# Kernel optimization log

Measured on AMD Instinct MI355X. Metric: run time of the kernel, lower is better.

Reference implementation:

```python
import jax, jax.numpy as jnp
import numpy as np

# ---- dims (see shape_source) ----
B, S = 1, 2048
D_MODEL, H, HD, RD = 2048, 16, 128, 64   # head_dim=128 (pow2 for Hadamard), rope dim 64
QLR = KVLR = 1024                        # lora ranks = d_model // 2
TOPK = 512
BLK = 32                                 # fp8 act-quant block size
FP8_MAX = 448.0                          # float8_e4m3 max
EPS = 1e-6


def linear(x, w, b):
    return x @ w.T + b


def rms_norm(x, w):
    return x * jax.lax.rsqrt(jnp.mean(x * x, axis=-1, keepdims=True) + EPS) * w


def rope_cos_sin(pos, d):
    half = d // 2
    inv = 1.0 / (10000.0 ** (jnp.arange(half, dtype=jnp.float32) / half))
    ang = pos[:, None].astype(jnp.float32) * inv[None, :]  # (s, half)
    return jnp.cos(ang), jnp.sin(ang)


def apply_rope(x, cos, sin):
    # rotate-half RoPE; cos/sin pre-broadcast to x's leading dims
    half = x.shape[-1] // 2
    x1, x2 = x[..., :half], x[..., half:]
    return jnp.concatenate([x1 * cos - x2 * sin, x2 * cos + x1 * sin], axis=-1)


def fwht(x):
    # fast Walsh-Hadamard transform over last dim (power of 2), scaled by d^-0.5
    d = x.shape[-1]
    lead = x.shape[:-1]
    h = 1
    while h < d:
        x = x.reshape(lead + (d // (2 * h), 2, h))
        x = jnp.concatenate([x[..., 0, :] + x[..., 1, :], x[..., 0, :] - x[..., 1, :]], axis=-1)
        x = x.reshape(lead + (d,))
        h *= 2
    return x * (d ** -0.5)


def act_quant_dequant(x):
    # block-scaled fp8 fake-quant: per-32-elem block, ue8m0 (power-of-2) scale, clamp to e4m3 range
    lead, d = x.shape[:-1], x.shape[-1]
    xb = x.reshape(lead + (d // BLK, BLK))
    amax = jnp.max(jnp.abs(xb), axis=-1)
    scale = jnp.exp2(jnp.ceil(jnp.log2(jnp.maximum(amax / FP8_MAX, 1e-12))))
    q = jnp.clip(xb / scale[..., None], -FP8_MAX, FP8_MAX)
    return (q * scale[..., None]).reshape(lead + (d,))


def setup_inputs() -> dict:
    key = jax.random.key(0)
    ks = iter(jax.random.split(key, 48))
    def W(o, i):
        return jax.random.normal(next(ks), (o, i), jnp.float32) * (i ** -0.5)
    def Bv(o):
        return jnp.zeros((o,), jnp.float32)
    return dict(
        x=jax.random.normal(next(ks), (B, S, D_MODEL), jnp.float32),
        start_pos=0,
        q_down_w=W(QLR, D_MODEL), q_down_b=Bv(QLR),
        q_norm_w=jnp.ones((QLR,), jnp.float32),
        q_nope_up_w=W(H * HD, QLR), q_nope_up_b=Bv(H * HD),
        q_rope_up_w=W(H * RD, QLR), q_rope_up_b=Bv(H * RD),
        kv_down_w=W(KVLR, D_MODEL), kv_down_b=Bv(KVLR),
        kv_norm_w=jnp.ones((KVLR,), jnp.float32),
        k_up_w=W(H * HD, KVLR), k_up_b=Bv(H * HD),
        v_up_w=W(H * HD, KVLR), v_up_b=Bv(H * HD),
        k_rope_w=W(RD, D_MODEL), k_rope_b=Bv(RD),
        out_w=W(D_MODEL, H * HD), out_b=Bv(D_MODEL),
        idx_q_w=W(H * HD, QLR), idx_q_b=Bv(H * HD),
        idx_k_w=W(HD, D_MODEL), idx_k_b=Bv(HD),
        idx_k_norm_w=jnp.ones((HD,), jnp.float32),
        idx_w_w=W(H, D_MODEL), idx_w_b=Bv(H),
    )


def reference(x, start_pos, q_down_w, q_down_b, q_norm_w, q_nope_up_w, q_nope_up_b,
              q_rope_up_w, q_rope_up_b, kv_down_w, kv_down_b, kv_norm_w,
              k_up_w, k_up_b, v_up_w, v_up_b, k_rope_w, k_rope_b, out_w, out_b,
              idx_q_w, idx_q_b, idx_k_w, idx_k_b, idx_k_norm_w, idx_w_w, idx_w_b):
    b, s, _ = x.shape
    pos = jnp.arange(start_pos, start_pos + s)
    cos_r, sin_r = rope_cos_sin(pos, RD)  # (s, RD/2)

    # --- MLA queries: low-rank down, RMSNorm, decoupled nope/rope up-proj ---
    q_c = rms_norm(linear(x, q_down_w, q_down_b), q_norm_w)            # (b,s,QLR)
    q_nope = linear(q_c, q_nope_up_w, q_nope_up_b).reshape(b, s, H, HD)
    q_rope = linear(q_c, q_rope_up_w, q_rope_up_b).reshape(b, s, H, RD)
    q_rope = apply_rope(q_rope, cos_r[:, None, :], sin_r[:, None, :])
    q = jnp.concatenate([q_nope, q_rope], axis=-1).transpose(0, 2, 1, 3)  # (b,H,s,HD+RD)

    # --- MLA keys/values: compressed kv + shared rope key ---
    kv_c = rms_norm(linear(x, kv_down_w, kv_down_b), kv_norm_w)        # (b,s,KVLR)
    k_pe = apply_rope(linear(x, k_rope_w, k_rope_b), cos_r, sin_r)     # (b,s,RD)
    k_nope = linear(kv_c, k_up_w, k_up_b).reshape(b, s, H, HD)
    v = linear(kv_c, v_up_w, v_up_b).reshape(b, s, H, HD).transpose(0, 2, 1, 3)
    k = jnp.concatenate(
        [k_nope, jnp.broadcast_to(k_pe[:, :, None, :], (b, s, H, RD))], axis=-1
    ).transpose(0, 2, 1, 3)                                            # (b,H,s,HD+RD)

    # --- lightning indexer: rotated, block-fp8-quantized scoring + top-k ---
    qi = linear(q_c, idx_q_w, idx_q_b).reshape(b, s, H, HD)
    ki = rms_norm(linear(x, idx_k_w, idx_k_b), idx_k_norm_w)           # (b,s,HD)
    qi_r = apply_rope(qi[..., :RD], cos_r[:, None, :], sin_r[:, None, :])
    ki_r = apply_rope(ki[..., :RD], cos_r, sin_r)
    qi = fwht(jnp.concatenate([qi[..., RD:], qi_r], axis=-1))          # rotate_activation
    ki = fwht(jnp.concatenate([ki[..., RD:], ki_r], axis=-1))
    qdq = act_quant_dequant(qi)                                        # (b,s,H,HD)
    kdq = act_quant_dequant(ki)                                        # (b,s,HD)
    w_idx = (x @ idx_w_w.T + idx_w_b) * (H ** -0.5)                    # (b,s,H)
    dots = jnp.einsum('bshd,btd->bsht', qdq, kdq)
    score = jnp.einsum('bsht,bsh->bst', jax.nn.relu(dots), w_idx) * (HD ** -0.5)
    _, topk_idx = jax.lax.top_k(score, min(TOPK, s))                   # (b,s,k)

    bi = jnp.arange(b)[:, None, None]
    si = jnp.arange(s)[None, :, None]
    index_mask = jnp.zeros((b, s, s), bool).at[bi, si, topk_idx].set(True)

    # --- sparse attention over selected tokens ---
    att = jnp.einsum('bhsd,bhtd->bhst', q, k) * ((HD + RD) ** -0.5)
    att = jnp.where(index_mask[:, None], att, jnp.float32(-1e30))
    att = jax.nn.softmax(att, axis=-1)
    o = jnp.einsum('bhst,bhtd->bhsd', att, v)
    o = o.transpose(0, 2, 1, 3).reshape(b, s, H * HD)
    return linear(o, out_w, out_b)
```

## Files before the change

kernel.cpp:

```cpp
#include <hip/hip_runtime.h>
#include <hip/hip_bf16.h>
#include <math.h>

#define S 2048
#define DM 2048
#define NH 16
#define HD 128
#define RD 64
#define LR 1024
#define TOPK 512

#define GT_M 128
#define GT_N 64
#define GT_K 16

__global__ __launch_bounds__(256)
void k_gemm(const float* __restrict__ A, const float* __restrict__ W,
            const float* __restrict__ bias, float* __restrict__ C,
            int M, int N, int K, float alpha)
{
    __shared__ float As[GT_K][GT_M + 4];
    __shared__ float Ws[GT_K][GT_N + 4];
    const int tid = threadIdx.x;
    const int tx = tid & 15, ty = tid >> 4;
    const int m0 = blockIdx.y * GT_M, n0 = blockIdx.x * GT_N;

    float acc[8][4];
#pragma unroll
    for (int i = 0; i < 8; ++i)
#pragma unroll
        for (int j = 0; j < 4; ++j) acc[i][j] = 0.f;

    const int ar = tid >> 1;
    const int ak = (tid & 1) << 3;
    const int wr = tid >> 2;
    const int wk = (tid & 3) << 2;

    for (int kk = 0; kk < K; kk += GT_K) {
        float4 v0 = *(const float4*)&A[(size_t)(m0 + ar) * K + kk + ak];
        float4 v1 = *(const float4*)&A[(size_t)(m0 + ar) * K + kk + ak + 4];
        float4 w0 = make_float4(0.f, 0.f, 0.f, 0.f);
        if (n0 + wr < N) w0 = *(const float4*)&W[(size_t)(n0 + wr) * K + kk + wk];
        __syncthreads();
        As[ak + 0][ar] = v0.x; As[ak + 1][ar] = v0.y; As[ak + 2][ar] = v0.z; As[ak + 3][ar] = v0.w;
        As[ak + 4][ar] = v1.x; As[ak + 5][ar] = v1.y; As[ak + 6][ar] = v1.z; As[ak + 7][ar] = v1.w;
        Ws[wk + 0][wr] = w0.x; Ws[wk + 1][wr] = w0.y; Ws[wk + 2][wr] = w0.z; Ws[wk + 3][wr] = w0.w;
        __syncthreads();
#pragma unroll
        for (int k = 0; k < GT_K; ++k) {
            float a0[8], b0[4];
            *(float4*)&a0[0] = *(const float4*)&As[k][ty * 8];
            *(float4*)&a0[4] = *(const float4*)&As[k][ty * 8 + 4];
            *(float4*)&b0[0] = *(const float4*)&Ws[k][tx * 4];
#pragma unroll
            for (int i = 0; i < 8; ++i)
#pragma unroll
                for (int j = 0; j < 4; ++j)
                    acc[i][j] = fmaf(a0[i], b0[j], acc[i][j]);
        }
    }
    const int n = n0 + tx * 4;
    if (n < N) {
#pragma unroll
        for (int i = 0; i < 8; ++i) {
            const int m = m0 + ty * 8 + i;
            float4 o;
            o.x = (acc[i][0] + bias[n + 0]) * alpha;
            o.y = (acc[i][1] + bias[n + 1]) * alpha;
            o.z = (acc[i][2] + bias[n + 2]) * alpha;
            o.w = (acc[i][3] + bias[n + 3]) * alpha;
            *(float4*)&C[(size_t)m * N + n] = o;
        }
    }
}

template<typename TA>
__global__ __launch_bounds__(256)
void k_gemm64(const TA* __restrict__ A, const float* __restrict__ W,
              const float* __restrict__ bias, double* __restrict__ C,
              int M, int N, int K, double alpha)
{
    __shared__ double As[16][66];
    __shared__ double Ws[16][66];
    const int tid = threadIdx.x;
    const int tx = tid & 15, ty = tid >> 4;
    const int m0 = blockIdx.y * 64, n0 = blockIdx.x * 64;
    const int r = tid >> 2, k4 = (tid & 3) << 2;

    double acc[4][4];
#pragma unroll
    for (int i = 0; i < 4; ++i)
#pragma unroll
        for (int j = 0; j < 4; ++j) acc[i][j] = 0.0;

    for (int kk = 0; kk < K; kk += 16) {
        double av[4], wv[4];
        const TA* ap = &A[(size_t)(m0 + r) * K + kk + k4];
#pragma unroll
        for (int i = 0; i < 4; ++i) av[i] = (double)ap[i];
        if (n0 + r < N) {
            const float* wp = &W[(size_t)(n0 + r) * K + kk + k4];
#pragma unroll
            for (int i = 0; i < 4; ++i) wv[i] = (double)wp[i];
        } else {
#pragma unroll
            for (int i = 0; i < 4; ++i) wv[i] = 0.0;
        }
        __syncthreads();
#pragma unroll
        for (int i = 0; i < 4; ++i) { As[k4 + i][r] = av[i]; Ws[k4 + i][r] = wv[i]; }
        __syncthreads();
#pragma unroll 4
        for (int k = 0; k < 16; ++k) {
            double a[4], b[4];
#pragma unroll
            for (int i = 0; i < 4; ++i) a[i] = As[k][ty * 4 + i];
#pragma unroll
            for (int j = 0; j < 4; ++j) b[j] = Ws[k][tx * 4 + j];
#pragma unroll
            for (int i = 0; i < 4; ++i)
#pragma unroll
                for (int j = 0; j < 4; ++j)
                    acc[i][j] = fma(a[i], b[j], acc[i][j]);
        }
    }
    const int n = n0 + tx * 4;
    if (n < N) {
#pragma unroll
        for (int i = 0; i < 4; ++i) {
            const int m = m0 + ty * 4 + i;
#pragma unroll
            for (int j = 0; j < 4; ++j)
                C[(size_t)m * N + n + j] = (acc[i][j] + (double)bias[n + j]) * alpha;
        }
    }
}

__global__ __launch_bounds__(256)
void k_rmsnorm(const float* __restrict__ X, const float* __restrict__ w,
               float* __restrict__ Y, int D)
{
    const int row = blockIdx.x;
    const float* x = X + (size_t)row * D;
    float* y = Y + (size_t)row * D;
    float ss = 0.f;
    for (int i = threadIdx.x; i < D; i += 256) { float v = x[i]; ss = fmaf(v, v, ss); }
#pragma unroll
    for (int m = 1; m < 64; m <<= 1) ss += __shfl_xor(ss, m, 64);
    __shared__ float red[4];
    if ((threadIdx.x & 63) == 0) red[threadIdx.x >> 6] = ss;
    __syncthreads();
    const float tot = red[0] + red[1] + red[2] + red[3];
    const float r = 1.0f / sqrtf(tot / (float)D + 1e-6f);
    for (int i = threadIdx.x; i < D; i += 256) y[i] = x[i] * r * w[i];
}

__global__ __launch_bounds__(256)
void k_rmsnorm64(const double* __restrict__ X, const float* __restrict__ w,
                 double* __restrict__ Y, int D)
{
    const int row = blockIdx.x;
    const double* x = X + (size_t)row * D;
    double* y = Y + (size_t)row * D;
    double ss = 0.0;
    for (int i = threadIdx.x; i < D; i += 256) { double v = x[i]; ss = fma(v, v, ss); }
#pragma unroll
    for (int m = 1; m < 64; m <<= 1) ss += __shfl_xor(ss, m, 64);
    __shared__ double red[4];
    if ((threadIdx.x & 63) == 0) red[threadIdx.x >> 6] = ss;
    __syncthreads();
    const double tot = red[0] + red[1] + red[2] + red[3];
    const double r = 1.0 / sqrt(tot / (double)D + 1e-6);
    for (int i = threadIdx.x; i < D; i += 256) y[i] = x[i] * r * (double)w[i];
}

__global__ __launch_bounds__(256)
void k_rope_table(const int* __restrict__ start_pos,
                  float* __restrict__ cos32, float* __restrict__ sin32)
{
    const int idx = blockIdx.x * 256 + threadIdx.x;
    if (idx >= S * 32) return;
    const int s = idx >> 5, j = idx & 31;
    const float posf = (float)(start_pos[0] + s);
    const double p64 = pow(10000.0, (double)j * 0.03125);
    const float p32 = (float)p64;
    const float inv32 = (float)(1.0 / (double)p32);
    const float ang = posf * inv32;
    cos32[idx] = (float)cos((double)ang);
    sin32[idx] = (float)sin((double)ang);
}

__global__ __launch_bounds__(256)
void k_rope_apply(float* __restrict__ X, const float* __restrict__ cosT,
                  const float* __restrict__ sinT, int heads)
{
    const int idx = blockIdx.x * 256 + threadIdx.x;
    if (idx >= S * heads * 32) return;
    const int j = idx & 31;
    const int vh = idx >> 5;
    const int s = vh / heads;
    const float c = cosT[s * 32 + j], sn = sinT[s * 32 + j];
    float* p = X + (size_t)vh * 64;
    const float x1 = p[j], x2 = p[32 + j];
    p[j]      = x1 * c - x2 * sn;
    p[32 + j] = x2 * c + x1 * sn;
}

__global__ __launch_bounds__(256)
void k_idx_prep64(double* __restrict__ X, const float* __restrict__ cosT,
                  const float* __restrict__ sinT, int heads, int nvec)
{
    const int wid = (int)((blockIdx.x * 256 + threadIdx.x) >> 6);
    const int lane = threadIdx.x & 63;
    if (wid >= nvec) return;
    const int s = wid / heads;
    double* x = X + (size_t)wid * 128;
    double y0, y1;
    if (lane < 32) {
        y0 = x[64 + 2 * lane]; y1 = x[64 + 2 * lane + 1];
    } else {
        const int j0 = (2 * (lane - 32)) & 31;
        const double a0 = x[j0], a1 = x[j0 + 1];
        const double b0 = x[j0 + 32], b1 = x[j0 + 33];
        const double c0 = (double)cosT[s * 32 + j0], c1 = (double)cosT[s * 32 + j0 + 1];
        const double s0 = (double)sinT[s * 32 + j0], s1 = (double)sinT[s * 32 + j0 + 1];
        if (lane < 48) { y0 = a0 * c0 - b0 * s0; y1 = a1 * c1 - b1 * s1; }
        else           { y0 = b0 * c0 + a0 * s0; y1 = b1 * c1 + a1 * s1; }
    }
    { const double t0 = y0 + y1, t1 = y0 - y1; y0 = t0; y1 = t1; }
#pragma unroll
    for (int m = 1; m < 64; m <<= 1) {
        const double p0 = __shfl_xor(y0, m, 64);
        const double p1 = __shfl_xor(y1, m, 64);
        if ((lane & m) == 0) { y0 = y0 + p0; y1 = y1 + p1; }
        else                 { y0 = p0 - y0; y1 = p1 - y1; }
    }
    const double SCL = 1.0 / sqrt(128.0);
    x[2 * lane] = y0 * SCL; x[2 * lane + 1] = y1 * SCL;
}

__global__ __launch_bounds__(256)
void k_score64(const double* __restrict__ QI, const double* __restrict__ KI,
               const double* __restrict__ Widx, double* __restrict__ SC)
{
    __shared__ double Qs[32][66];
    __shared__ double Ks[32][66];
    const int tid = threadIdx.x;
    const int tx = tid & 15, ty = tid >> 4;
    const int s0 = blockIdx.y * 64, t0 = blockIdx.x * 64;
    const int r = tid >> 2, k8 = (tid & 3) << 3;

    double sc[4][4];
#pragma unroll
    for (int i = 0; i < 4; ++i)
#pragma unroll
        for (int j = 0; j < 4; ++j) sc[i][j] = 0.0;

    for (int h = 0; h < NH; ++h) {
        double dot[4][4];
#pragma unroll
        for (int i = 0; i < 4; ++i)
#pragma unroll
            for (int j = 0; j < 4; ++j) dot[i][j] = 0.0;
        for (int kk = 0; kk < HD; kk += 32) {
            __syncthreads();
            {
                const double* qp = &QI[((size_t)(s0 + r) * NH + h) * HD + kk + k8];
                const double* kp = &KI[(size_t)(t0 + r) * HD + kk + k8];
#pragma unroll
                for (int i = 0; i < 8; ++i) { Qs[k8 + i][r] = qp[i]; Ks[k8 + i][r] = kp[i]; }
            }
            __syncthreads();
#pragma unroll 8
            for (int k = 0; k < 32; ++k) {
                double a[4], b[4];
#pragma unroll
                for (int i = 0; i < 4; ++i) a[i] = Qs[k][ty * 4 + i];
#pragma unroll
                for (int j = 0; j < 4; ++j) b[j] = Ks[k][tx * 4 + j];
#pragma unroll
                for (int i = 0; i < 4; ++i)
#pragma unroll
                    for (int j = 0; j < 4; ++j)
                        dot[i][j] = fma(a[i], b[j], dot[i][j]);
            }
        }
#pragma unroll
        for (int i = 0; i < 4; ++i) {
            const double w = Widx[(size_t)(s0 + ty * 4 + i) * NH + h];
#pragma unroll
            for (int j = 0; j < 4; ++j)
                sc[i][j] = fma(fmax(dot[i][j], 0.0), w, sc[i][j]);
        }
    }
    const double SCL = 1.0 / sqrt(128.0);
#pragma unroll
    for (int i = 0; i < 4; ++i)
#pragma unroll
        for (int j = 0; j < 4; ++j)
            SC[(size_t)(s0 + ty * 4 + i) * S + t0 + tx * 4 + j] = sc[i][j] * SCL;
}

__global__ __launch_bounds__(256)
void k_topk64(const double* __restrict__ SC, unsigned* __restrict__ Mask)
{
    __shared__ unsigned long long u[S];
    __shared__ int cnt_sh, cg_sh, ce_sh, cut_sh;
    const int tid = threadIdx.x;
    const int row = blockIdx.x;
    for (int j = tid; j < S; j += 256) {
        unsigned long long b = (unsigned long long)__double_as_longlong(SC[(size_t)row * S + j]);
        if (b == 0x8000000000000000ull) b = 0ull;
        u[j] = (b & 0x8000000000000000ull) ? ~b : (b | 0x8000000000000000ull);
    }
    __syncthreads();
    unsigned long long lo = 0ull, hi = ~0ull;
    for (int it = 0; it < 64 && lo < hi; ++it) {
        const unsigned long long mid = lo + ((hi - lo) >> 1) + 1ull;
        if (tid == 0) cnt_sh = 0;
        __syncthreads();
        int c = 0;
        for (int j = tid; j < S; j += 256) c += (u[j] >= mid) ? 1 : 0;
#pragma unroll
        for (int m = 1; m < 64; m <<= 1) c += __shfl_xor(c, m, 64);
        if ((tid & 63) == 0) atomicAdd(&cnt_sh, c);
        __syncthreads();
        const int cge = cnt_sh;
        __syncthreads();
        if (cge >= TOPK) lo = mid; else hi = mid - 1ull;
    }
    const unsigned long long T = lo;
    if (tid == 0) { cg_sh = 0; ce_sh = 0; }
    __syncthreads();
    int cg = 0, ce = 0;
    for (int j = tid; j < S; j += 256) {
        cg += (u[j] > T) ? 1 : 0; ce += (u[j] == T) ? 1 : 0;
    }
#pragma unroll
    for (int m = 1; m < 64; m <<= 1) { cg += __shfl_xor(cg, m, 64); ce += __shfl_xor(ce, m, 64); }
    if ((tid & 63) == 0) { atomicAdd(&cg_sh, cg); atomicAdd(&ce_sh, ce); }
    __syncthreads();
    if (tid == 0) {
        const int need = TOPK - cg_sh;
        int cut = S - 1;
        if (ce_sh != need) {
            int acc = 0; cut = -1;
            for (int t = 0; t < S; ++t)
                if (u[t] == T) { ++acc; if (acc == need) { cut = t; break; } }
        }
        cut_sh = cut;
    }
    __syncthreads();
    const int cut = cut_sh;
    for (int w = tid; w < S / 32; w += 256) {
        unsigned bits = 0u;
#pragma unroll 4
        for (int b = 0; b < 32; ++b) {
            const int j = w * 32 + b;
            const bool sel = (u[j] > T) || ((u[j] == T) && (j <= cut));
            bits |= (sel ? 1u : 0u) << b;
        }
        Mask[(size_t)row * (S / 32) + w] = bits;
    }
}

__global__ __launch_bounds__(256)
void k_attn(const float* __restrict__ QN, const float* __restrict__ QR,
            const float* __restrict__ KN, const float* __restrict__ KP,
            const float* __restrict__ V, const unsigned* __restrict__ Mask,
            float* __restrict__ O)
{
    __shared__ float AB[2 * 64 * 68];
    __shared__ float Ps[64][68];
    const int tid = threadIdx.x;
    const int tx = tid & 15, ty = tid >> 4;
    const int h = blockIdx.y;
    const int s0 = blockIdx.x * 64;
    const int r = tid >> 2;
    const int c4 = (tid & 3) << 2;

    float o[4][8];
    float mrow[4], lrow[4];
#pragma unroll
    for (int i = 0; i < 4; ++i) {
        mrow[i] = -INFINITY; lrow[i] = 0.f;
#pragma unroll
        for (int jd = 0; jd < 8; ++jd) o[i][jd] = 0.f;
    }

    for (int t0 = 0; t0 < S; t0 += 64) {
        float lg[4][4];
#pragma unroll
        for (int i = 0; i < 4; ++i)
#pragma unroll
            for (int j = 0; j < 4; ++j) lg[i][j] = 0.f;

        for (int c = 0; c < 3; ++c) {
            __syncthreads();
#pragma unroll
            for (int jj = 0; jj < 4; ++jj) {
                const int kk = c4 + 16 * jj;
                float4 va, vb;
                if (c < 2) {
                    va = *(const float4*)&QN[((size_t)(s0 + r) * NH + h) * HD + c * 64 + kk];
                    vb = *(const float4*)&KN[((size_t)(t0 + r) * NH + h) * HD + c * 64 + kk];
                } else {
                    va = *(const float4*)&QR[((size_t)(s0 + r) * NH + h) * RD + kk];
                    vb = *(const float4*)&KP[(size_t)(t0 + r) * RD + kk];
                }
                AB[(kk + 0) * 68 + r] = va.x; AB[(kk + 1) * 68 + r] = va.y;
                AB[(kk + 2) * 68 + r] = va.z; AB[(kk + 3) * 68 + r] = va.w;
                AB[4352 + (kk + 0) * 68 + r] = vb.x; AB[4352 + (kk + 1) * 68 + r] = vb.y;
                AB[4352 + (kk + 2) * 68 + r] = vb.z; AB[4352 + (kk + 3) * 68 + r] = vb.w;
            }
            __syncthreads();
#pragma unroll 16
            for (int k = 0; k < 64; ++k) {
                float a[4], b[4];
                *(float4*)a = *(const float4*)&AB[k * 68 + ty * 4];
                *(float4*)b = *(const float4*)&AB[4352 + k * 68 + tx * 4];
#pragma unroll
                for (int i = 0; i < 4; ++i)
#pragma unroll
                    for (int j = 0; j < 4; ++j)
                        lg[i][j] = fmaf(a[i], b[j], lg[i][j]);
            }
        }
        __syncthreads();

        float p[4][4], mt[4], alpha[4], psum[4];
#pragma unroll
        for (int i = 0; i < 4; ++i) {
            mt[i] = -INFINITY;
            const unsigned mw = Mask[(size_t)(s0 + 4 * ty + i) * (S / 32) + (t0 >> 5) + (tx >> 3)];
            const unsigned nib = (mw >> ((tx & 7) << 2)) & 0xFu;
#pragma unroll
            for (int j = 0; j < 4; ++j) {
                if ((nib >> j) & 1u) {
                    const float l = lg[i][j] * 0.07216878364870323f;
                    p[i][j] = l;
                    mt[i] = fmaxf(mt[i], l);
                } else p[i][j] = -INFINITY;
            }
        }
#pragma unroll
        for (int m = 1; m < 16; m <<= 1)
#pragma unroll
            for (int i = 0; i < 4; ++i) mt[i] = fmaxf(mt[i], __shfl_xor(mt[i], m, 64));
#pragma unroll
        for (int i = 0; i < 4; ++i) {
            const float mnew = fmaxf(mrow[i], mt[i]);
            alpha[i] = (mnew == -INFINITY) ? 1.f : expf(mrow[i] - mnew);
            mrow[i] = mnew;
            psum[i] = 0.f;
            float pj[4];
#pragma unroll
            for (int j = 0; j < 4; ++j) {
                const float pv = (p[i][j] == -INFINITY) ? 0.f : expf(p[i][j] - mnew);
                pj[j] = pv; psum[i] += pv;
            }
            *(float4*)&Ps[4 * ty + i][tx * 4] = make_float4(pj[0], pj[1], pj[2], pj[3]);
        }
#pragma unroll
        for (int m = 1; m < 16; m <<= 1)
#pragma unroll
            for (int i = 0; i < 4; ++i) psum[i] += __shfl_xor(psum[i], m, 64);
#pragma unroll
        for (int i = 0; i < 4; ++i) {
            lrow[i] = lrow[i] * alpha[i] + psum[i];
#pragma unroll
            for (int jd = 0; jd < 8; ++jd) o[i][jd] *= alpha[i];
        }
#pragma unroll
        for (int jj = 0; jj < 8; ++jj) {
            const int dq = c4 + 16 * jj;
            float4 vv = *(const float4*)&V[((size_t)(t0 + r) * NH + h) * HD + dq];
            AB[r * 128 + dq + 0] = vv.x; AB[r * 128 + dq + 1] = vv.y;
            AB[r * 128 + dq + 2] = vv.z; AB[r * 128 + dq + 3] = vv.w;
        }
        __syncthreads();
#pragma unroll 4
        for (int tc = 0; tc < 64; ++tc) {
            float pv[4];
#pragma unroll
            for (int i = 0; i < 4; ++i) pv[i] = Ps[4 * ty + i][tc];
#pragma unroll
            for (int jd = 0; jd < 8; ++jd) {
                const float vvv = AB[tc * 128 + tx + 16 * jd];
#pragma unroll
                for (int i = 0; i < 4; ++i) o[i][jd] = fmaf(pv[i], vvv, o[i][jd]);
            }
        }
    }
#pragma unroll
    for (int i = 0; i < 4; ++i) {
        const float inv = 1.0f / lrow[i];
#pragma unroll
        for (int jd = 0; jd < 8; ++jd)
            O[((size_t)(s0 + 4 * ty + i) * NH + h) * HD + tx + 16 * jd] = o[i][jd] * inv;
    }
}

__global__ __launch_bounds__(256)
void k_cast64to32(const double* __restrict__ X, float* __restrict__ Y, int n)
{
    const int i = blockIdx.x * 256 + threadIdx.x;
    if (i < n) Y[i] = (float)X[i];
}

extern "C" void kernel_launch(void* const* d_in, const int* in_sizes, int n_in,
                              void* d_out, int out_size, void* d_ws, size_t ws_size,
                              hipStream_t stream)
{
    const float* x            = (const float*)d_in[0];
    const int*   start_pos    = (const int*)  d_in[1];
    const float* q_down_w     = (const float*)d_in[2];
    const float* q_down_b     = (const float*)d_in[3];
    const float* q_norm_w     = (const float*)d_in[4];
    const float* q_nope_up_w  = (const float*)d_in[5];
    const float* q_nope_up_b  = (const float*)d_in[6];
    const float* q_rope_up_w  = (const float*)d_in[7];
    const float* q_rope_up_b  = (const float*)d_in[8];
    const float* kv_down_w    = (const float*)d_in[9];
    const float* kv_down_b    = (const float*)d_in[10];
    const float* kv_norm_w    = (const float*)d_in[11];
    const float* k_up_w       = (const float*)d_in[12];
    const float* k_up_b       = (const float*)d_in[13];
    const float* v_up_w       = (const float*)d_in[14];
    const float* v_up_b       = (const float*)d_in[15];
    const float* k_rope_w     = (const float*)d_in[16];
    const float* k_rope_b     = (const float*)d_in[17];
    const float* out_w        = (const float*)d_in[18];
    const float* out_b        = (const float*)d_in[19];
    const float* idx_q_w      = (const float*)d_in[20];
    const float* idx_q_b      = (const float*)d_in[21];
    const float* idx_k_w      = (const float*)d_in[22];
    const float* idx_k_b      = (const float*)d_in[23];
    const float* idx_k_norm_w = (const float*)d_in[24];
    const float* idx_w_w      = (const float*)d_in[25];
    const float* idx_w_b      = (const float*)d_in[26];

    char* base = (char*)d_ws;
    size_t off = 0;
    auto alloc = [&](size_t bytes) -> void* {
        void* p = base + off; off += (bytes + 255) & ~(size_t)255; return p;
    };

    double* score64 = (double*)alloc((size_t)S * S * 8);
    double* q_c64   = score64;
    double* qi64    = (double*)alloc((size_t)S * NH * HD * 8);
    double* ki64    = (double*)alloc((size_t)S * HD * 8);
    double* widx64  = (double*)alloc((size_t)S * NH * 8);
    unsigned* Mask  = (unsigned*)alloc((size_t)S * (S / 32) * 4);
    float* q_c32    = (float*)alloc((size_t)S * LR * 4);
    float* kv_c     = (float*)alloc((size_t)S * LR * 4);
    float* qn       = (float*)alloc((size_t)S * NH * HD * 4);
    float* qr       = (float*)alloc((size_t)S * NH * RD * 4);
    float* kn       = (float*)alloc((size_t)S * NH * HD * 4);
    float* vv       = (float*)alloc((size_t)S * NH * HD * 4);
    float* kpe      = (float*)alloc((size_t)S * RD * 4);
    float* cos32    = (float*)alloc((size_t)S * 32 * 4);
    float* sin32    = (float*)alloc((size_t)S * 32 * 4);
    float* obuf     = q_c32;

    dim3 blk(256);
    k_rope_table<<<dim3(S * 32 / 256), blk, 0, stream>>>(start_pos, cos32, sin32);

    k_gemm64<float><<<dim3(LR / 64, S / 64), blk, 0, stream>>>(x, q_down_w, q_down_b, q_c64, S, LR, DM, 1.0);
    k_rmsnorm64<<<dim3(S), blk, 0, stream>>>(q_c64, q_norm_w, q_c64, LR);
    k_cast64to32<<<dim3(S * LR / 256), blk, 0, stream>>>(q_c64, q_c32, S * LR);
    k_gemm64<double><<<dim3(NH * HD / 64, S / 64), blk, 0, stream>>>(q_c64, idx_q_w, idx_q_b, qi64, S, NH * HD, LR, 1.0);
    k_gemm64<float><<<dim3(HD / 64, S / 64), blk, 0, stream>>>(x, idx_k_w, idx_k_b, ki64, S, HD, DM, 1.0);
    k_rmsnorm64<<<dim3(S), blk, 0, stream>>>(ki64, idx_k_norm_w, ki64, HD);
    k_gemm64<float><<<dim3(1, S / 64), blk, 0, stream>>>(x, idx_w_w, idx_w_b, widx64, S, NH, DM, 0.25);
    k_idx_prep64<<<dim3(S * NH / 4), blk, 0, stream>>>(qi64, cos32, sin32, NH, S * NH);
    k_idx_prep64<<<dim3(S / 4), blk, 0, stream>>>(ki64, cos32, sin32, 1, S);
    k_score64<<<dim3(S / 64, S / 64), blk, 0, stream>>>(qi64, ki64, widx64, score64);
    k_topk64<<<dim3(S), blk, 0, stream>>>(score64, Mask);

    k_gemm<<<dim3(LR / GT_N, S / GT_M), blk, 0, stream>>>(x, kv_down_w, kv_down_b, kv_c, S, LR, DM, 1.f);
    k_rmsnorm<<<dim3(S), blk, 0, stream>>>(kv_c, kv_norm_w, kv_c, LR);
    k_gemm<<<dim3(1, S / GT_M), blk, 0, stream>>>(x, k_rope_w, k_rope_b, kpe, S, RD, DM, 1.f);
    k_gemm<<<dim3(NH * HD / GT_N, S / GT_M), blk, 0, stream>>>(q_c32, q_nope_up_w, q_nope_up_b, qn, S, NH * HD, LR, 1.f);
    k_gemm<<<dim3(NH * RD / GT_N, S / GT_M), blk, 0, stream>>>(q_c32, q_rope_up_w, q_rope_up_b, qr, S, NH * RD, LR, 1.f);
    k_gemm<<<dim3(NH * HD / GT_N, S / GT_M), blk, 0, stream>>>(kv_c, k_up_w, k_up_b, kn, S, NH * HD, LR, 1.f);
    k_gemm<<<dim3(NH * HD / GT_N, S / GT_M), blk, 0, stream>>>(kv_c, v_up_w, v_up_b, vv, S, NH * HD, LR, 1.f);
    k_rope_apply<<<dim3(S * NH * 32 / 256), blk, 0, stream>>>(qr, cos32, sin32, NH);
    k_rope_apply<<<dim3(S * 32 / 256), blk, 0, stream>>>(kpe, cos32, sin32, 1);
    k_attn<<<dim3(S / 64, NH), blk, 0, stream>>>(qn, qr, kn, kpe, vv, Mask, obuf);
    k_gemm<<<dim3(DM / GT_N, S / GT_M), blk, 0, stream>>>(obuf, out_w, out_b, (float*)d_out, S, DM, NH * HD, 1.f);
}
```

Measured before the change: 3.426 ms.

## Run fp32 projection GEMMs on bf16 MFMA with split hi/lo emulation

Adds a GEMM kernel that splits each fp32 operand into high and low bf16 parts and accumulates three MFMA products (hi*hi, lo*hi, hi*lo), giving near-fp32 accuracy on the matrix cores. It uses 128x128 tiles with XOR-swizzled shared memory. The new kernel replaces the scalar FMA fp32 GEMM for the kv down-projection, the q/k/v up-projections and the output projection. Conversion happens on every tile load, and dropping the lo*lo term introduces a small precision loss.

```diff
diff --git a/kernel.cpp b/kernel.cpp
--- a/kernel.cpp
+++ b/kernel.cpp
@@ -9,6 +9,14 @@
 #define RD 64
 #define LR 1024
 #define TOPK 512
+
+typedef __attribute__((ext_vector_type(8))) short bf16x8;
+typedef __attribute__((ext_vector_type(4))) float f32x4;
+
+__device__ __forceinline__ unsigned short bf16h(float x) {
+    __hip_bfloat16 b = __float2bfloat16(x);
+    return *reinterpret_cast<unsigned short*>(&b);
+}
 
 #define GT_M 128
 #define GT_N 64
@@ -72,6 +80,89 @@
             *(float4*)&C[(size_t)m * N + n] = o;
         }
     }
+}
+
+__global__ __launch_bounds__(256)
+void k_gemm_bf16s(const float* __restrict__ A, const float* __restrict__ W,
+                  const float* __restrict__ bias, float* __restrict__ C,
+                  int M, int N, int K, float alpha)
+{
+    __shared__ unsigned short AhS[128 * 32], AlS[128 * 32], WhS[128 * 32], WlS[128 * 32];
+    const int tid = threadIdx.x;
+    const int wid = tid >> 6, lane = tid & 63;
+    const int wm = (wid >> 1) * 64, wn = (wid & 1) * 64;
+    const int m0 = blockIdx.y * 128, n0 = blockIdx.x * 128;
+    const int lrow = lane & 15, lkg = lane >> 4;
+
+    f32x4 acc[4][4];
+    const f32x4 zero = {0.f, 0.f, 0.f, 0.f};
+#pragma unroll
+    for (int mt = 0; mt < 4; ++mt)
+#pragma unroll
+        for (int nt = 0; nt < 4; ++nt) acc[mt][nt] = zero;
+
+    for (int kk = 0; kk < K; kk += 32) {
+        __syncthreads();
+#pragma unroll
+        for (int c = 0; c < 2; ++c) {
+            const int chunk = tid + (c << 8);
+            const int row = chunk >> 2, kg = chunk & 3;
+            const int uidx = ((((row << 6) + (kg << 4)) ^ ((row & 7) << 4)) >> 1);
+            const float* ap = &A[(size_t)(m0 + row) * K + kk + (kg << 3)];
+            const float* wp = &W[(size_t)(n0 + row) * K + kk + (kg << 3)];
+            float4 av0 = *(const float4*)ap; float4 av1 = *(const float4*)(ap + 4);
+            float4 wv0 = *(const float4*)wp; float4 wv1 = *(const float4*)(wp + 4);
+            float as[8] = {av0.x, av0.y, av0.z, av0.w, av1.x, av1.y, av1.z, av1.w};
+            float ws[8] = {wv0.x, wv0.y, wv0.z, wv0.w, wv1.x, wv1.y, wv1.z, wv1.w};
+            bf16x8 ah, al, wh, wl;
+#pragma unroll
+            for (int i = 0; i < 8; ++i) {
+                unsigned short h = bf16h(as[i]);
+                float hf = __uint_as_float((unsigned)h << 16);
+                ah[i] = (short)h; al[i] = (short)bf16h(as[i] - hf);
+                unsigned short g = bf16h(ws[i]);
+                float gf = __uint_as_float((unsigned)g << 16);
+                wh[i] = (short)g; wl[i] = (short)bf16h(ws[i] - gf);
+            }
+            *(bf16x8*)&AhS[uidx] = ah; *(bf16x8*)&AlS[uidx] = al;
+            *(bf16x8*)&WhS[uidx] = wh; *(bf16x8*)&WlS[uidx] = wl;
+        }
+        __syncthreads();
+
+        bf16x8 whf[4], wlf[4];
+#pragma unroll
+        for (int nt = 0; nt < 4; ++nt) {
+            const int row = wn + nt * 16 + lrow;
+            const int u = ((((row << 6) + (lkg << 4)) ^ ((row & 7) << 4)) >> 1);
+            whf[nt] = *(const bf16x8*)&WhS[u];
+            wlf[nt] = *(const bf16x8*)&WlS[u];
+        }
+#pragma unroll
+        for (int mt = 0; mt < 4; ++mt) {
+            const int row = wm + mt * 16 + lrow;
+            const int u = ((((row << 6) + (lkg << 4)) ^ ((row & 7) << 4)) >> 1);
+            bf16x8 ahf = *(const bf16x8*)&AhS[u];
+            bf16x8 alf = *(const bf16x8*)&AlS[u];
+#pragma unroll
+            for (int nt = 0; nt < 4; ++nt) {
+                acc[mt][nt] = __builtin_amdgcn_mfma_f32_16x16x32_bf16(ahf, whf[nt], acc[mt][nt], 0, 0, 0);
+                acc[mt][nt] = __builtin_amdgcn_mfma_f32_16x16x32_bf16(alf, whf[nt], acc[mt][nt], 0, 0, 0);
+                acc[mt][nt] = __builtin_amdgcn_mfma_f32_16x16x32_bf16(ahf, wlf[nt], acc[mt][nt], 0, 0, 0);
+            }
+        }
+    }
+
+#pragma unroll
+    for (int mt = 0; mt < 4; ++mt)
+#pragma unroll
+        for (int nt = 0; nt < 4; ++nt) {
+            const int col = n0 + wn + nt * 16 + lrow;
+            const float b = bias[col];
+            const int rbase = m0 + wm + mt * 16 + (lkg << 2);
+#pragma unroll
+            for (int r = 0; r < 4; ++r)
+                C[(size_t)(rbase + r) * N + col] = (acc[mt][nt][r] + b) * alpha;
+        }
 }
 
 template<typename TA>
@@ -578,15 +669,15 @@
     k_score64<<<dim3(S / 64, S / 64), blk, 0, stream>>>(qi64, ki64, widx64, score64);
     k_topk64<<<dim3(S), blk, 0, stream>>>(score64, Mask);
 
-    k_gemm<<<dim3(LR / GT_N, S / GT_M), blk, 0, stream>>>(x, kv_down_w, kv_down_b, kv_c, S, LR, DM, 1.f);
+    k_gemm_bf16s<<<dim3(LR / 128, S / 128), blk, 0, stream>>>(x, kv_down_w, kv_down_b, kv_c, S, LR, DM, 1.f);
     k_rmsnorm<<<dim3(S), blk, 0, stream>>>(kv_c, kv_norm_w, kv_c, LR);
     k_gemm<<<dim3(1, S / GT_M), blk, 0, stream>>>(x, k_rope_w, k_rope_b, kpe, S, RD, DM, 1.f);
-    k_gemm<<<dim3(NH * HD / GT_N, S / GT_M), blk, 0, stream>>>(q_c32, q_nope_up_w, q_nope_up_b, qn, S, NH * HD, LR, 1.f);
-    k_gemm<<<dim3(NH * RD / GT_N, S / GT_M), blk, 0, stream>>>(q_c32, q_rope_up_w, q_rope_up_b, qr, S, NH * RD, LR, 1.f);
-    k_gemm<<<dim3(NH * HD / GT_N, S / GT_M), blk, 0, stream>>>(kv_c, k_up_w, k_up_b, kn, S, NH * HD, LR, 1.f);
-    k_gemm<<<dim3(NH * HD / GT_N, S / GT_M), blk, 0, stream>>>(kv_c, v_up_w, v_up_b, vv, S, NH * HD, LR, 1.f);
+    k_gemm_bf16s<<<dim3(NH * HD / 128, S / 128), blk, 0, stream>>>(q_c32, q_nope_up_w, q_nope_up_b, qn, S, NH * HD, LR, 1.f);
+    k_gemm_bf16s<<<dim3(NH * RD / 128, S / 128), blk, 0, stream>>>(q_c32, q_rope_up_w, q_rope_up_b, qr, S, NH * RD, LR, 1.f);
+    k_gemm_bf16s<<<dim3(NH * HD / 128, S / 128), blk, 0, stream>>>(kv_c, k_up_w, k_up_b, kn, S, NH * HD, LR, 1.f);
+    k_gemm_bf16s<<<dim3(NH * HD / 128, S / 128), blk, 0, stream>>>(kv_c, v_up_w, v_up_b, vv, S, NH * HD, LR, 1.f);
     k_rope_apply<<<dim3(S * NH * 32 / 256), blk, 0, stream>>>(qr, cos32, sin32, NH);
     k_rope_apply<<<dim3(S * 32 / 256), blk, 0, stream>>>(kpe, cos32, sin32, 1);
     k_attn<<<dim3(S / 64, NH), blk, 0, stream>>>(qn, qr, kn, kpe, vv, Mask, obuf);
-    k_gemm<<<dim3(DM / GT_N, S / GT_M), blk, 0, stream>>>(obuf, out_w, out_b, (float*)d_out, S, DM, NH * HD, 1.f);
-}
+    k_gemm_bf16s<<<dim3(DM / 128, S / 128), blk, 0, stream>>>(obuf, out_w, out_b, (float*)d_out, S, DM, NH * HD, 1.f);
+}
```

Result: faster. 3.069 ms (-10.4%).
